# Kernel optimization log

Hardware: AMD Instinct MI355X
Metric: run time of the kernel (lower is better)

Reference implementation:

```python
import jax, jax.numpy as jnp
import numpy as np

N = 100000
E = 1600000
IN_DIM = 128
HID = 128
OUT = 64
BN_EPS = 1e-5


def setup_inputs() -> dict:
    key = jax.random.key(0)
    ks = jax.random.split(key, 12)
    x = jax.random.normal(ks[0], (N, IN_DIM), dtype=jnp.float32)
    src = jax.random.randint(ks[1], (E,), 0, N, dtype=jnp.int64)
    dst = jax.random.randint(ks[2], (E,), 0, N, dtype=jnp.int64)
    edge_index = jnp.stack([src, dst], axis=0)
    def glorot(k, fan_in, fan_out):
        s = jnp.sqrt(6.0 / (fan_in + fan_out)).astype(jnp.float32)
        return jax.random.uniform(k, (fan_in, fan_out), jnp.float32, -s, s)
    return {
        "x": x,
        "edge_index": edge_index,
        "W1": glorot(ks[3], IN_DIM, HID), "b1": jnp.zeros((HID,), jnp.float32),
        "g1": jnp.ones((HID,), jnp.float32), "be1": jnp.zeros((HID,), jnp.float32),
        "W2": glorot(ks[4], HID, HID), "b2": jnp.zeros((HID,), jnp.float32),
        "g2": jnp.ones((HID,), jnp.float32), "be2": jnp.zeros((HID,), jnp.float32),
        "W3": glorot(ks[5], HID, OUT), "b3": jnp.zeros((OUT,), jnp.float32),
    }


def _gcn_norm(edge_index, n):
    # PyG GCNConv: add self-loops, symmetric normalization D^-1/2 (A+I) D^-1/2
    loop = jnp.arange(n, dtype=edge_index.dtype)
    src = jnp.concatenate([edge_index[0], loop])
    dst = jnp.concatenate([edge_index[1], loop])
    deg = jax.ops.segment_sum(jnp.ones_like(src, dtype=jnp.float32), dst, num_segments=n)
    dinv = jnp.where(deg > 0, jax.lax.rsqrt(deg), 0.0)
    norm = dinv[src] * dinv[dst]  # [E+N]
    return src, dst, norm


def _gcn(x, src, dst, norm, W, b, n):
    xw = x @ W                                  # [N, out]
    msg = xw[src] * norm[:, None]               # gather over edges
    return jax.ops.segment_sum(msg, dst, num_segments=n) + b


def _bn(x, g, be):
    # training-mode BatchNorm1d over node dim, biased variance
    mu = jnp.mean(x, axis=0)
    var = jnp.mean(jnp.square(x - mu), axis=0)
    return (x - mu) * jax.lax.rsqrt(var + BN_EPS) * g + be


def reference(x, edge_index, W1, b1, g1, be1, W2, b2, g2, be2, W3, b3):
    n = x.shape[0]
    src, dst, norm = _gcn_norm(edge_index, n)
    h = _gcn(x, src, dst, norm, W1, b1, n)
    h = jax.nn.relu(_bn(h, g1, be1))  # dropout = identity (eval)
    h = _gcn(h, src, dst, norm, W2, b2, n)
    h = jax.nn.relu(_bn(h, g2, be2))
    return _gcn(h, src, dst, norm, W3, b3, n)
```

## Files before the change

kernel.cpp:

```cpp
#include <hip/hip_runtime.h>
#include <cstdint>
#include <cstddef>

#define BN_EPS 1e-5f
#define BKT 256
#define BSH 9
#define CHUNK 8192

typedef __attribute__((ext_vector_type(8))) short bf16x8;
typedef __attribute__((ext_vector_type(4))) float f32x4;

__device__ __forceinline__ unsigned int f32_to_bf16_rne(float f) {
    unsigned int u = __float_as_uint(f);
    u += 0x7FFFu + ((u >> 16) & 1u);
    return u >> 16;
}
__device__ __forceinline__ unsigned int pack_bf16x2(float a, float b) {
    return f32_to_bf16_rne(a) | (f32_to_bf16_rne(b) << 16);
}
__device__ __forceinline__ float bf16_lo(unsigned int p) { return __uint_as_float(p << 16); }
__device__ __forceinline__ float bf16_hi(unsigned int p) { return __uint_as_float(p & 0xFFFF0000u); }

__global__ void hist_kernel(const int* __restrict__ dst, int* __restrict__ H, int e, int G) {
    __shared__ int h[BKT];
    int t = threadIdx.x, g = blockIdx.x;
    h[t] = 0;
    __syncthreads();
    int base = g * CHUNK;
#pragma unroll
    for (int i = 0; i < CHUNK / 256; i++) {
        int idx = base + i * 256 + t;
        if (idx < e) atomicAdd(&h[dst[idx] >> BSH], 1);
    }
    __syncthreads();
    H[t * G + g] = h[t];
}

__global__ void bin_scatter_kernel(const int* __restrict__ src, const int* __restrict__ dst,
                                   const int* __restrict__ Hscan, uint2* __restrict__ binned,
                                   int e, int G) {
    __shared__ int cur[BKT];
    int t = threadIdx.x, g = blockIdx.x;
    cur[t] = Hscan[t * G + g];
    __syncthreads();
    int base = g * CHUNK;
#pragma unroll
    for (int i = 0; i < CHUNK / 256; i++) {
        int idx = base + i * 256 + t;
        if (idx < e) {
            int s = src[idx], d = dst[idx];
            int pos = atomicAdd(&cur[d >> BSH], 1);
            uint2 v; v.x = (unsigned)s; v.y = (unsigned)d;
            binned[pos] = v;
        }
    }
}

__global__ __launch_bounds__(256) void bucket_build_kernel(const uint2* __restrict__ binned,
                                                           const int* __restrict__ Hscan,
                                                           int* __restrict__ cnt,
                                                           int* __restrict__ rowptr,
                                                           float* __restrict__ dinv,
                                                           int* __restrict__ esrc,
                                                           int e, int G, int n) {
    __shared__ int lcnt[512], lexc[512], ssum[256];
    const int t = threadIdx.x;
    const int b = blockIdx.x;
    const int start = Hscan[b * G];
    const int end = (b == BKT - 1) ? e : Hscan[(b + 1) * G];

    lcnt[t] = 0; lcnt[t + 256] = 0;
    __syncthreads();
    for (int i = start + t; i < end; i += 256)
        atomicAdd(&lcnt[binned[i].y & 511], 1);
    __syncthreads();

    int a0 = lcnt[2 * t], a1 = lcnt[2 * t + 1];
    ssum[t] = a0 + a1;
    __syncthreads();
    for (int off = 1; off < 256; off <<= 1) {
        int v = (t >= off) ? ssum[t - off] : 0;
        __syncthreads();
        ssum[t] += v;
        __syncthreads();
    }
    int excl = (t == 0) ? 0 : ssum[t - 1];
    lexc[2 * t] = excl;
    lexc[2 * t + 1] = excl + a0;
    __syncthreads();

    int nodebase = b << BSH;
#pragma unroll
    for (int j2 = 0; j2 < 2; j2++) {
        int j = 2 * t + j2;
        int node = nodebase + j;
        if (node < n) {
            int c = lcnt[j];
            cnt[node] = c;
            rowptr[node] = start + lexc[j];
            dinv[node] = rsqrtf((float)(c + 1));
        }
    }
    __syncthreads();

    for (int i = start + t; i < end; i += 256) {
        uint2 ed = binned[i];
        int pos = start + atomicAdd(&lexc[ed.y & 511], 1);
        esrc[pos] = (int)ed.x;
    }
}


__global__ void blocksum_kernel(const int* __restrict__ in, int* __restrict__ bsum, int n) {
    int t = threadIdx.x;
    int base = blockIdx.x * 1024 + t * 4;
    int s = 0;
    if (base + 3 < n) {
        int4 v = *(const int4*)&in[base];
        s = v.x + v.y + v.z + v.w;
    } else {
        for (int j = 0; j < 4; j++) if (base + j < n) s += in[base + j];
    }
    __shared__ int ls[256];
    ls[t] = s;
    __syncthreads();
    for (int off = 128; off > 0; off >>= 1) {
        if (t < off) ls[t] += ls[t + off];
        __syncthreads();
    }
    if (t == 0) bsum[blockIdx.x] = ls[0];
}

__global__ void scan_bsum_kernel(int* __restrict__ bsum, int nb) {
    int t = threadIdx.x;
    __shared__ int ls[256];
    int v = (t < nb) ? bsum[t] : 0;
    ls[t] = v;
    __syncthreads();
    for (int off = 1; off < 256; off <<= 1) {
        int p = (t >= off) ? ls[t - off] : 0;
        __syncthreads();
        ls[t] += p;
        __syncthreads();
    }
    if (t < nb) bsum[t] = ls[t] - v;
}

__global__ void scan_write1_kernel(const int* __restrict__ in, const int* __restrict__ bsum,
                                   int* __restrict__ out, int n) {
    int t = threadIdx.x;
    int base = blockIdx.x * 1024 + t * 4;
    int v[4];
    int s = 0;
    if (base + 3 < n) {
        int4 q = *(const int4*)&in[base];
        v[0] = q.x; v[1] = q.y; v[2] = q.z; v[3] = q.w;
        s = q.x + q.y + q.z + q.w;
    } else {
        for (int j = 0; j < 4; j++) { v[j] = (base + j < n) ? in[base + j] : 0; s += v[j]; }
    }
    __shared__ int ls[256];
    ls[t] = s;
    __syncthreads();
    for (int off = 1; off < 256; off <<= 1) {
        int p = (t >= off) ? ls[t - off] : 0;
        __syncthreads();
        ls[t] += p;
        __syncthreads();
    }
    int run = bsum[blockIdx.x] + ls[t] - s;
    if (base + 3 < n) {
        int4 r; r.x = run; r.y = run + v[0]; r.z = run + v[0] + v[1]; r.w = run + v[0] + v[1] + v[2];
        *(int4*)&out[base] = r;
    } else {
        for (int j = 0; j < 4; j++) {
            if (base + j < n) out[base + j] = run;
            run += v[j];
        }
    }
}


template <int OUTC>
__global__ void wprep_kernel(const float* __restrict__ W,
                             uint4* __restrict__ whi, uint4* __restrict__ wlo) {
    constexpr int NSLOT = (OUTC / 16) * 4 * 64;
    int slot = blockIdx.x * 256 + threadIdx.x;
    if (slot >= NSLOT) return;
    int l  = slot & 63;
    int kc = (slot >> 6) & 3;
    int ct = slot >> 8;
    int c  = ct * 16 + (l & 15);
    int k0 = kc * 32 + (l >> 4) * 8;
    unsigned hi[4], lo[4];
#pragma unroll
    for (int jj = 0; jj < 4; jj++) {
        float v0 = W[(size_t)(k0 + 2 * jj) * OUTC + c];
        float v1 = W[(size_t)(k0 + 2 * jj + 1) * OUTC + c];
        unsigned h0 = f32_to_bf16_rne(v0), h1 = f32_to_bf16_rne(v1);
        float l0 = v0 - __uint_as_float(h0 << 16);
        float l1 = v1 - __uint_as_float(h1 << 16);
        hi[jj] = h0 | (h1 << 16);
        lo[jj] = pack_bf16x2(l0, l1);
    }
    uint4 uh; uh.x = hi[0]; uh.y = hi[1]; uh.z = hi[2]; uh.w = hi[3];
    uint4 ul; ul.x = lo[0]; ul.y = lo[1]; ul.z = lo[2]; ul.w = lo[3];
    whi[slot] = uh;
    wlo[slot] = ul;
}


template <int OUTC>
__global__ __launch_bounds__(256) void gemm_kernel(const float* __restrict__ X,
                                                   const uint4* __restrict__ whi,
                                                   const uint4* __restrict__ wlo,
                                                   const float* __restrict__ scale,
                                                   const float* __restrict__ shift,
                                                   const float* __restrict__ dinv,
                                                   unsigned int* __restrict__ Y, int n) {
    constexpr int NCT = OUTC / 16;
    constexpr int CTW = NCT / 4;
    __shared__ __align__(16) unsigned short lAhi[64 * 128];
    __shared__ __align__(16) unsigned short lAlo[64 * 128];
    __shared__ float ldv[64];
    const int t = threadIdx.x;
    const int base = blockIdx.x * 64;
    const int lane = t & 63;
    const int w = t >> 6;
    const bool bn = (scale != nullptr);

    if (t < 64) { int r = base + t; ldv[t] = (r < n) ? dinv[r] : 0.0f; }

    bf16x8 bhi[CTW][4], blo[CTW][4];
#pragma unroll
    for (int c = 0; c < CTW; c++) {
        int ct = w * CTW + c;
#pragma unroll
        for (int kc = 0; kc < 4; kc++) {
            int slot = (ct * 4 + kc) * 64 + lane;
            bhi[c][kc] = *reinterpret_cast<const bf16x8*>(whi + slot);
            blo[c][kc] = *reinterpret_cast<const bf16x8*>(wlo + slot);
        }
    }

    const int col4 = (t & 31) * 4;
    float4 sc4, sh4;
    if (bn) {
        sc4 = *(const float4*)&scale[col4];
        sh4 = *(const float4*)&shift[col4];
    }
#pragma unroll
    for (int i = 0; i < 8; i++) {
        int row = i * 8 + (t >> 5);
        int r = base + row;
        float4 xv = make_float4(0.f, 0.f, 0.f, 0.f);
        if (r < n) xv = *(const float4*)&X[(size_t)r * 128 + col4];
        if (bn) {
            xv.x = fmaxf(fmaf(xv.x, sc4.x, sh4.x), 0.0f);
            xv.y = fmaxf(fmaf(xv.y, sc4.y, sh4.y), 0.0f);
            xv.z = fmaxf(fmaf(xv.z, sc4.z, sh4.z), 0.0f);
            xv.w = fmaxf(fmaf(xv.w, sc4.w, sh4.w), 0.0f);
        }
        unsigned h0 = f32_to_bf16_rne(xv.x), h1 = f32_to_bf16_rne(xv.y);
        unsigned h2 = f32_to_bf16_rne(xv.z), h3 = f32_to_bf16_rne(xv.w);
        float l0 = xv.x - __uint_as_float(h0 << 16);
        float l1 = xv.y - __uint_as_float(h1 << 16);
        float l2 = xv.z - __uint_as_float(h2 << 16);
        float l3 = xv.w - __uint_as_float(h3 << 16);
        uint2 ph; ph.x = h0 | (h1 << 16); ph.y = h2 | (h3 << 16);
        uint2 pl; pl.x = pack_bf16x2(l0, l1); pl.y = pack_bf16x2(l2, l3);
        int off = row * 256 + ((col4 * 2) ^ ((row & 7) << 4));
        *(uint2*)((char*)lAhi + off) = ph;
        *(uint2*)((char*)lAlo + off) = pl;
    }
    __syncthreads();

    const int arow = lane & 15;
    const int kb16 = (lane >> 4) * 16;
#pragma unroll
    for (int rt = 0; rt < 4; rt++) {
        f32x4 acc[CTW];
#pragma unroll
        for (int c = 0; c < CTW; c++) acc[c] = (f32x4){0.f, 0.f, 0.f, 0.f};
        int row = rt * 16 + arow;
        int rb = row * 256;
        int sw = (row & 7) << 4;
#pragma unroll
        for (int kc = 0; kc < 4; kc++) {
            int off = rb + ((kc * 64 + kb16) ^ sw);
            bf16x8 ah = *(const bf16x8*)((const char*)lAhi + off);
            bf16x8 al = *(const bf16x8*)((const char*)lAlo + off);
#pragma unroll
            for (int c = 0; c < CTW; c++) {
                acc[c] = __builtin_amdgcn_mfma_f32_16x16x32_bf16(bhi[c][kc], ah, acc[c], 0, 0, 0);
                acc[c] = __builtin_amdgcn_mfma_f32_16x16x32_bf16(blo[c][kc], ah, acc[c], 0, 0, 0);
                acc[c] = __builtin_amdgcn_mfma_f32_16x16x32_bf16(bhi[c][kc], al, acc[c], 0, 0, 0);
            }
        }
        int r = base + row;
        if (r < n) {
            float dv = ldv[row];
#pragma unroll
            for (int c = 0; c < CTW; c++) {
                int ct = w * CTW + c;
                uint2 o;
                o.x = pack_bf16x2(acc[c][0] * dv, acc[c][1] * dv);
                o.y = pack_bf16x2(acc[c][2] * dv, acc[c][3] * dv);
                *(uint2*)&Y[(size_t)r * (OUTC / 2) + ct * 8 + (lane >> 4) * 2] = o;
            }
        }
    }
}


__global__ __launch_bounds__(256) void agg128_kernel(const unsigned int* __restrict__ xw,
                                                     const int* __restrict__ rowptr,
                                                     const int* __restrict__ cnt,
                                                     const int* __restrict__ esrc,
                                                     const float* __restrict__ dinv,
                                                     const float* __restrict__ bias,
                                                     float* __restrict__ out, int n) {
    const uint2* xw2 = (const uint2*)xw;
    int wid = (blockIdx.x * 256 + threadIdx.x) >> 6;
    int lane = threadIdx.x & 63;
    int half = lane >> 5;
    int hl = lane & 31;
    int node = wid * 2 + half;
    bool ok = node < n;
    int nc = ok ? node : 0;

    float di = dinv[nc];
    int beg = rowptr[nc];
    int cv  = ok ? cnt[nc] : 0;
    int last = beg + cv - 1;
    int nb = (cv + 7) >> 3;

    uint2 ap = xw2[(size_t)nc * 32 + hl];
    float ax = bf16_lo(ap.x), ay = bf16_hi(ap.x);
    float az = bf16_lo(ap.y), aw = bf16_hi(ap.y);

    int s[8], sn[8];
    if (nb > 0) {
#pragma unroll
        for (int j = 0; j < 8; j++) {
            int idx = beg + j;
            s[j] = esrc[idx <= last ? idx : last];
        }
    }
    for (int b = 0; b < nb; b++) {
        int ebase = beg + b * 8;
        if (b + 1 < nb) {
#pragma unroll
            for (int j = 0; j < 8; j++) {
                int idx = ebase + 8 + j;
                sn[j] = esrc[idx <= last ? idx : last];
            }
        }
        uint2 v[8];
#pragma unroll
        for (int j = 0; j < 8; j++) v[j] = xw2[(size_t)s[j] * 32 + hl];
        int rem = last - ebase;
#pragma unroll
        for (int j = 0; j < 8; j++) {
            float m = (j <= rem) ? 1.0f : 0.0f;
            ax = fmaf(m, bf16_lo(v[j].x), ax);
            ay = fmaf(m, bf16_hi(v[j].x), ay);
            az = fmaf(m, bf16_lo(v[j].y), az);
            aw = fmaf(m, bf16_hi(v[j].y), aw);
        }
        if (b + 1 < nb) {
#pragma unroll
            for (int j = 0; j < 8; j++) s[j] = sn[j];
        }
    }
    if (ok) {
        float4 bv = ((const float4*)bias)[hl];
        float4 o;
        o.x = fmaf(di, ax, bv.x);
        o.y = fmaf(di, ay, bv.y);
        o.z = fmaf(di, az, bv.z);
        o.w = fmaf(di, aw, bv.w);
        ((float4*)(out + (size_t)node * 128))[hl] = o;
    }
}


__global__ __launch_bounds__(256) void agg64_kernel(const unsigned int* __restrict__ xw,
                                                    const int* __restrict__ rowptr,
                                                    const int* __restrict__ cnt,
                                                    const int* __restrict__ esrc,
                                                    const float* __restrict__ dinv,
                                                    const float* __restrict__ bias,
                                                    float* __restrict__ out, int n) {
    int wid = (blockIdx.x * 256 + threadIdx.x) >> 6;
    int lane = threadIdx.x & 63;
    int half = lane >> 5;
    int hl = lane & 31;
    int node = wid * 2 + half;
    bool ok = node < n;
    int nc = ok ? node : 0;

    float di = dinv[nc];
    int beg = rowptr[nc];
    int cv  = ok ? cnt[nc] : 0;
    int last = beg + cv - 1;
    int nb = (cv + 7) >> 3;

    unsigned int ap = xw[(size_t)nc * 32 + hl];
    float ax = bf16_lo(ap), ay = bf16_hi(ap);

    int s[8], sn[8];
    if (nb > 0) {
#pragma unroll
        for (int j = 0; j < 8; j++) {
            int idx = beg + j;
            s[j] = esrc[idx <= last ? idx : last];
        }
    }
    for (int b = 0; b < nb; b++) {
        int ebase = beg + b * 8;
        if (b + 1 < nb) {
#pragma unroll
            for (int j = 0; j < 8; j++) {
                int idx = ebase + 8 + j;
                sn[j] = esrc[idx <= last ? idx : last];
            }
        }
        unsigned int v[8];
#pragma unroll
        for (int j = 0; j < 8; j++) v[j] = xw[(size_t)s[j] * 32 + hl];
        int rem = last - ebase;
#pragma unroll
        for (int j = 0; j < 8; j++) {
            float m = (j <= rem) ? 1.0f : 0.0f;
            ax = fmaf(m, bf16_lo(v[j]), ax);
            ay = fmaf(m, bf16_hi(v[j]), ay);
        }
        if (b + 1 < nb) {
#pragma unroll
            for (int j = 0; j < 8; j++) s[j] = sn[j];
        }
    }
    if (ok) {
        float2 bv = ((const float2*)bias)[hl];
        float2 o;
        o.x = fmaf(di, ax, bv.x);
        o.y = fmaf(di, ay, bv.y);
        ((float2*)(out + (size_t)node * 64))[hl] = o;
    }
}


__global__ void bn_stats_kernel(const float* __restrict__ h, float* __restrict__ sums, int n) {
    int c = threadIdx.x & 127;
    int half = threadIdx.x >> 7;
    float s = 0.0f, q = 0.0f;
    for (int r = blockIdx.x * 2 + half; r < n; r += gridDim.x * 2) {
        float v = h[(size_t)r * 128 + c];
        s += v;
        q = fmaf(v, v, q);
    }
    __shared__ float ls[256], lq[256];
    ls[threadIdx.x] = s; lq[threadIdx.x] = q;
    __syncthreads();
    if (half == 0) {
        s += ls[c + 128];
        q += lq[c + 128];
        atomicAdd(&sums[c], s);
        atomicAdd(&sums[128 + c], q);
    }
}

__global__ void bn_finalize_kernel(const float* __restrict__ sums, const float* __restrict__ g,
                                   const float* __restrict__ be, float* __restrict__ scale,
                                   float* __restrict__ shift, int n) {
    int c = threadIdx.x;
    float inv_n = 1.0f / (float)n;
    float mean = sums[c] * inv_n;
    float var = sums[128 + c] * inv_n - mean * mean;
    float rstd = rsqrtf(var + BN_EPS);
    float sc = rstd * g[c];
    scale[c] = sc;
    shift[c] = be[c] - mean * sc;
}


extern "C" void kernel_launch(void* const* d_in, const int* in_sizes, int n_in,
                              void* d_out, int out_size, void* d_ws, size_t ws_size,
                              hipStream_t stream) {
    const float* x   = (const float*)d_in[0];
    const int*   ei  = (const int*)d_in[1];
    const float* W1  = (const float*)d_in[2];
    const float* b1  = (const float*)d_in[3];
    const float* g1  = (const float*)d_in[4];
    const float* be1 = (const float*)d_in[5];
    const float* W2  = (const float*)d_in[6];
    const float* b2  = (const float*)d_in[7];
    const float* g2  = (const float*)d_in[8];
    const float* be2 = (const float*)d_in[9];
    const float* W3  = (const float*)d_in[10];
    const float* b3  = (const float*)d_in[11];

    const int n = in_sizes[0] / 128;
    const int E = in_sizes[1] / 2;
    const int* srcv = ei;
    const int* dstv = ei + E;

    const int G = (E + CHUNK - 1) / CHUNK;
    const int HN = BKT * G;
    const int NB = (n + 511) >> 9;

    char* p = (char*)d_ws;
    auto carve = [&](size_t bytes) -> char* {
        char* q = p;
        p += (bytes + 255) & ~(size_t)255;
        return q;
    };
    int*   cnt    = (int*)carve((size_t)n * 4);
    int*   rowptr = (int*)carve((size_t)n * 4);
    float* dinv   = (float*)carve((size_t)n * 4);
    int*   esrc   = (int*)carve((size_t)E * 4);
    uint2* binned = (uint2*)carve((size_t)E * 8);
    int*   H      = (int*)carve((size_t)HN * 4);
    int*   Hscan  = (int*)carve((size_t)HN * 4);
    float* sums   = (float*)carve(512 * 4);
    float* bnsc   = (float*)carve(512 * 4);
    int*   bsum   = (int*)carve(1024 * 4);
    uint4* w1hi   = (uint4*)carve(2048 * 16);
    uint4* w1lo   = (uint4*)carve(2048 * 16);
    uint4* w2hi   = (uint4*)carve(2048 * 16);
    uint4* w2lo   = (uint4*)carve(2048 * 16);
    uint4* w3hi   = (uint4*)carve(1024 * 16);
    uint4* w3lo   = (uint4*)carve(1024 * 16);
    unsigned int* xwb = (unsigned int*)carve((size_t)n * 128 * 2);
    float* bufB   = (float*)carve((size_t)n * 128 * 4);

    hipMemsetAsync(sums, 0, 512 * 4, stream);

    int sbH = (HN + 1023) / 1024;

    wprep_kernel<128><<<8, 256, 0, stream>>>(W1, w1hi, w1lo);
    wprep_kernel<128><<<8, 256, 0, stream>>>(W2, w2hi, w2lo);
    wprep_kernel<64><<<4, 256, 0, stream>>>(W3, w3hi, w3lo);

    hist_kernel<<<G, 256, 0, stream>>>(dstv, H, E, G);
    blocksum_kernel<<<sbH, 256, 0, stream>>>(H, bsum, HN);
    scan_bsum_kernel<<<1, 256, 0, stream>>>(bsum, sbH);
    scan_write1_kernel<<<sbH, 256, 0, stream>>>(H, bsum, Hscan, HN);
    bin_scatter_kernel<<<G, 256, 0, stream>>>(srcv, dstv, Hscan, binned, E, G);
    bucket_build_kernel<<<NB, 256, 0, stream>>>(binned, Hscan, cnt, rowptr, dinv, esrc, E, G, n);

    int gb = (n + 63) / 64;
    int ab = (n + 7) / 8;

    gemm_kernel<128><<<gb, 256, 0, stream>>>(x, w1hi, w1lo, nullptr, nullptr, dinv, xwb, n);
    agg128_kernel<<<ab, 256, 0, stream>>>(xwb, rowptr, cnt, esrc, dinv, b1, bufB, n);
    bn_stats_kernel<<<512, 256, 0, stream>>>(bufB, sums, n);
    bn_finalize_kernel<<<1, 128, 0, stream>>>(sums, g1, be1, bnsc, bnsc + 128, n);

    gemm_kernel<128><<<gb, 256, 0, stream>>>(bufB, w2hi, w2lo, bnsc, bnsc + 128, dinv, xwb, n);
    agg128_kernel<<<ab, 256, 0, stream>>>(xwb, rowptr, cnt, esrc, dinv, b2, bufB, n);
    bn_stats_kernel<<<512, 256, 0, stream>>>(bufB, sums + 256, n);
    bn_finalize_kernel<<<1, 128, 0, stream>>>(sums + 256, g2, be2, bnsc + 256, bnsc + 384, n);

    gemm_kernel<64><<<gb, 256, 0, stream>>>(bufB, w3hi, w3lo, bnsc + 256, bnsc + 384, dinv, xwb, n);
    agg64_kernel<<<ab, 256, 0, stream>>>(xwb, rowptr, cnt, esrc, dinv, b3, (float*)d_out, n);
}
```

Measured before the change: 471.4 us.

## Fuse BatchNorm statistics into aggregation kernel and merge weight prep launches

Each agg128 block now accumulates per-channel sum and sum of squares in shared memory with LDS atomics. It then adds them into one of 8 strided global partial slots. A single small kernel reduces those partials and computes scale and shift. This removes the separate bn_stats pass that reread the full 100000x128 float buffer, and it merges three weight-prep launches into one. In exchange it adds LDS atomic contention, extra syncs in the aggregation kernel, and heavy global atomic traffic on only 2048 addresses across about 12500 blocks.

```diff
diff --git a/kernel.cpp b/kernel.cpp
--- a/kernel.cpp
+++ b/kernel.cpp
@@ -181,12 +181,9 @@
 }
 
 
-template <int OUTC>
-__global__ void wprep_kernel(const float* __restrict__ W,
-                             uint4* __restrict__ whi, uint4* __restrict__ wlo) {
-    constexpr int NSLOT = (OUTC / 16) * 4 * 64;
-    int slot = blockIdx.x * 256 + threadIdx.x;
-    if (slot >= NSLOT) return;
+__device__ __forceinline__ void wprep_one(const float* __restrict__ W,
+                                          uint4* __restrict__ whi, uint4* __restrict__ wlo,
+                                          int slot, int OUTC) {
     int l  = slot & 63;
     int kc = (slot >> 6) & 3;
     int ct = slot >> 8;
@@ -207,6 +204,15 @@
     uint4 ul; ul.x = lo[0]; ul.y = lo[1]; ul.z = lo[2]; ul.w = lo[3];
     whi[slot] = uh;
     wlo[slot] = ul;
+}
+
+__global__ void wprep_all_kernel(const float* __restrict__ W1, uint4* w1hi, uint4* w1lo,
+                                 const float* __restrict__ W2, uint4* w2hi, uint4* w2lo,
+                                 const float* __restrict__ W3, uint4* w3hi, uint4* w3lo) {
+    int id = blockIdx.x * 256 + threadIdx.x;
+    if (id < 2048)       wprep_one(W1, w1hi, w1lo, id, 128);
+    else if (id < 4096)  wprep_one(W2, w2hi, w2lo, id - 2048, 128);
+    else if (id < 5120)  wprep_one(W3, w3hi, w3lo, id - 4096, 64);
 }
 
 
@@ -319,7 +325,11 @@
                                                      const int* __restrict__ esrc,
                                                      const float* __restrict__ dinv,
                                                      const float* __restrict__ bias,
-                                                     float* __restrict__ out, int n) {
+                                                     float* __restrict__ out,
+                                                     float* __restrict__ bnpart, int n) {
+    __shared__ float lsum[256];
+    lsum[threadIdx.x] = 0.0f;
+
     const uint2* xw2 = (const uint2*)xw;
     int wid = (blockIdx.x * 256 + threadIdx.x) >> 6;
     int lane = threadIdx.x & 63;
@@ -373,15 +383,31 @@
             for (int j = 0; j < 8; j++) s[j] = sn[j];
         }
     }
+
+    float4 o = make_float4(0.f, 0.f, 0.f, 0.f);
     if (ok) {
         float4 bv = ((const float4*)bias)[hl];
-        float4 o;
         o.x = fmaf(di, ax, bv.x);
         o.y = fmaf(di, ay, bv.y);
         o.z = fmaf(di, az, bv.z);
         o.w = fmaf(di, aw, bv.w);
         ((float4*)(out + (size_t)node * 128))[hl] = o;
     }
+
+    __syncthreads();
+    if (ok) {
+        int c = hl * 4;
+        atomicAdd(&lsum[c + 0], o.x);
+        atomicAdd(&lsum[c + 1], o.y);
+        atomicAdd(&lsum[c + 2], o.z);
+        atomicAdd(&lsum[c + 3], o.w);
+        atomicAdd(&lsum[128 + c + 0], o.x * o.x);
+        atomicAdd(&lsum[128 + c + 1], o.y * o.y);
+        atomicAdd(&lsum[128 + c + 2], o.z * o.z);
+        atomicAdd(&lsum[128 + c + 3], o.w * o.w);
+    }
+    __syncthreads();
+    atomicAdd(&bnpart[(blockIdx.x & 7) * 256 + threadIdx.x], lsum[threadIdx.x]);
 }
 
 
@@ -451,37 +477,25 @@
 }
 
 
-__global__ void bn_stats_kernel(const float* __restrict__ h, float* __restrict__ sums, int n) {
-    int c = threadIdx.x & 127;
-    int half = threadIdx.x >> 7;
-    float s = 0.0f, q = 0.0f;
-    for (int r = blockIdx.x * 2 + half; r < n; r += gridDim.x * 2) {
-        float v = h[(size_t)r * 128 + c];
-        s += v;
-        q = fmaf(v, v, q);
-    }
-    __shared__ float ls[256], lq[256];
-    ls[threadIdx.x] = s; lq[threadIdx.x] = q;
-    __syncthreads();
-    if (half == 0) {
-        s += ls[c + 128];
-        q += lq[c + 128];
-        atomicAdd(&sums[c], s);
-        atomicAdd(&sums[128 + c], q);
-    }
-}
-
-__global__ void bn_finalize_kernel(const float* __restrict__ sums, const float* __restrict__ g,
-                                   const float* __restrict__ be, float* __restrict__ scale,
-                                   float* __restrict__ shift, int n) {
-    int c = threadIdx.x;
-    float inv_n = 1.0f / (float)n;
-    float mean = sums[c] * inv_n;
-    float var = sums[128 + c] * inv_n - mean * mean;
-    float rstd = rsqrtf(var + BN_EPS);
-    float sc = rstd * g[c];
-    scale[c] = sc;
-    shift[c] = be[c] - mean * sc;
+__global__ void bnred_kernel(const float* __restrict__ part, const float* __restrict__ g,
+                             const float* __restrict__ be, float* __restrict__ scale,
+                             float* __restrict__ shift, int n) {
+    int t = threadIdx.x;
+    float s = 0.0f;
+#pragma unroll
+    for (int k = 0; k < 8; k++) s += part[k * 256 + t];
+    __shared__ float L[256];
+    L[t] = s;
+    __syncthreads();
+    if (t < 128) {
+        float inv_n = 1.0f / (float)n;
+        float mean = L[t] * inv_n;
+        float var = L[128 + t] * inv_n - mean * mean;
+        float rstd = rsqrtf(var + BN_EPS);
+        float sc = rstd * g[t];
+        scale[t] = sc;
+        shift[t] = be[t] - mean * sc;
+    }
 }
 
 
@@ -523,7 +537,7 @@
     uint2* binned = (uint2*)carve((size_t)E * 8);
     int*   H      = (int*)carve((size_t)HN * 4);
     int*   Hscan  = (int*)carve((size_t)HN * 4);
-    float* sums   = (float*)carve(512 * 4);
+    float* bnpart = (float*)carve(2 * 8 * 256 * 4);
     float* bnsc   = (float*)carve(512 * 4);
     int*   bsum   = (int*)carve(1024 * 4);
     uint4* w1hi   = (uint4*)carve(2048 * 16);
@@ -535,13 +549,11 @@
     unsigned int* xwb = (unsigned int*)carve((size_t)n * 128 * 2);
     float* bufB   = (float*)carve((size_t)n * 128 * 4);
 
-    hipMemsetAsync(sums, 0, 512 * 4, stream);
+    hipMemsetAsync(bnpart, 0, 2 * 8 * 256 * 4, stream);
 
     int sbH = (HN + 1023) / 1024;
 
-    wprep_kernel<128><<<8, 256, 0, stream>>>(W1, w1hi, w1lo);
-    wprep_kernel<128><<<8, 256, 0, stream>>>(W2, w2hi, w2lo);
-    wprep_kernel<64><<<4, 256, 0, stream>>>(W3, w3hi, w3lo);
+    wprep_all_kernel<<<20, 256, 0, stream>>>(W1, w1hi, w1lo, W2, w2hi, w2lo, W3, w3hi, w3lo);
 
     hist_kernel<<<G, 256, 0, stream>>>(dstv, H, E, G);
     blocksum_kernel<<<sbH, 256, 0, stream>>>(H, bsum, HN);
@@ -554,14 +566,12 @@
     int ab = (n + 7) / 8;
 
     gemm_kernel<128><<<gb, 256, 0, stream>>>(x, w1hi, w1lo, nullptr, nullptr, dinv, xwb, n);
-    agg128_kernel<<<ab, 256, 0, stream>>>(xwb, rowptr, cnt, esrc, dinv, b1, bufB, n);
-    bn_stats_kernel<<<512, 256, 0, stream>>>(bufB, sums, n);
-    bn_finalize_kernel<<<1, 128, 0, stream>>>(sums, g1, be1, bnsc, bnsc + 128, n);
+    agg128_kernel<<<ab, 256, 0, stream>>>(xwb, rowptr, cnt, esrc, dinv, b1, bufB, bnpart, n);
+    bnred_kernel<<<1, 256, 0, stream>>>(bnpart, g1, be1, bnsc, bnsc + 128, n);
 
     gemm_kernel<128><<<gb, 256, 0, stream>>>(bufB, w2hi, w2lo, bnsc, bnsc + 128, dinv, xwb, n);
-    agg128_kernel<<<ab, 256, 0, stream>>>(xwb, rowptr, cnt, esrc, dinv, b2, bufB, n);
-    bn_stats_kernel<<<512, 256, 0, stream>>>(bufB, sums + 256, n);
-    bn_finalize_kernel<<<1, 128, 0, stream>>>(sums + 256, g2, be2, bnsc + 256, bnsc + 384, n);
+    agg128_kernel<<<ab, 256, 0, stream>>>(xwb, rowptr, cnt, esrc, dinv, b2, bufB, bnpart + 2048, n);
+    bnred_kernel<<<1, 256, 0, stream>>>(bnpart + 2048, g2, be2, bnsc + 256, bnsc + 384, n);
 
     gemm_kernel<64><<<gb, 256, 0, stream>>>(bufB, w3hi, w3lo, bnsc + 256, bnsc + 384, dinv, xwb, n);
     agg64_kernel<<<ab, 256, 0, stream>>>(xwb, rowptr, cnt, esrc, dinv, b3, (float*)d_out, n);
```

Result: slower. 580.8 us (+23.2%).
